# Kernel optimization log

Measured on AMD Instinct MI355X. Metric: run time of the kernel, lower is better.

The kernel has to match this reference:

```python
import jax, jax.numpy as jnp
import numpy as np
from jax import lax

B, C, H, W = 16, 128, 96, 96  # dim = C


def conv2d(x, w, b, pad, groups=1):
    y = lax.conv_general_dilated(
        x, w, window_strides=(1, 1), padding=[(pad, pad), (pad, pad)],
        dimension_numbers=("NCHW", "OIHW", "NCHW"), feature_group_count=groups)
    return y + b[None, :, None, None]


def setup_inputs() -> dict:
    key = jax.random.key(0)
    ks = jax.random.split(key, 16)
    std = 0.02
    inp = {
        "x": jax.random.normal(ks[0], (B, C, H, W), jnp.float32),
        "sin": jax.random.normal(ks[1], (H * W, C), jnp.float32),
        "cos": jax.random.normal(ks[2], (H * W, C), jnp.float32),
        # qkvo: 1x1 conv, dim -> 4*dim
        "w_qkvo": jax.random.normal(ks[3], (4 * C, C, 1, 1), jnp.float32) * std,
        "b_qkvo": jnp.zeros((4 * C,), jnp.float32),
        # lepe: 5x5 depthwise conv
        "w_lepe": jax.random.normal(ks[4], (C, 1, 5, 5), jnp.float32) * std,
        "b_lepe": jnp.zeros((C,), jnp.float32),
        # proj: 1x1 conv
        "w_proj": jax.random.normal(ks[5], (C, C, 1, 1), jnp.float32) * std,
        "b_proj": jnp.zeros((C,), jnp.float32),
        # 3x3 depthwise convs on q/k/v
        "w_q": jax.random.normal(ks[6], (C, 1, 3, 3), jnp.float32) * std,
        "b_q": jnp.zeros((C,), jnp.float32),
        "w_k": jax.random.normal(ks[7], (C, 1, 3, 3), jnp.float32) * std,
        "b_k": jnp.zeros((C,), jnp.float32),
        "w_v": jax.random.normal(ks[8], (C, 1, 3, 3), jnp.float32) * std,
        "b_v": jnp.zeros((C,), jnp.float32),
    }
    return inp


def reference(x, sin, cos, w_qkvo, b_qkvo, w_lepe, b_lepe, w_proj, b_proj,
              w_q, b_q, w_k, b_k, w_v, b_v):
    # sin/cos are accepted but unused, matching the original forward.
    b, c, h, w = x.shape
    hw = h * w
    scale = c ** (-0.5)

    qkvo = conv2d(x, w_qkvo, b_qkvo, 0)          # (B, 4C, H, W)
    qkv = qkvo[:, :3 * c]
    o = qkvo[:, 3 * c:]
    lepe = conv2d(qkv[:, 2 * c:], w_lepe, b_lepe, 2, groups=c)  # (B, C, H, W)

    q = qkv[:, :c]
    k = qkv[:, c:2 * c]
    v = qkv[:, 2 * c:]
    q = q + conv2d(q, w_q, b_q, 1, groups=c)
    k = k + conv2d(k, w_k, b_k, 1, groups=c)
    v = v + conv2d(v, w_v, b_v, 1, groups=c)

    # (B, C, H, W) -> (B, HW, C)
    to_tok = lambda t: t.reshape(b, c, hw).transpose(0, 2, 1)
    q = jax.nn.elu(to_tok(q)) + 1.0
    k = jax.nn.elu(to_tok(k)) + 1.0
    v = to_tok(v)

    k_mean = k.mean(axis=1, keepdims=True)                    # (B, 1, C)
    z = jnp.einsum("bnc,bmc->bnm", q, k_mean) * scale         # (B, HW, 1)

    s = (scale / hw) ** 0.5
    kv = jnp.einsum("bnc,bnd->bcd", k * s, v * s)             # (B, C, C)

    res = (jnp.einsum("bnc,bcd->bnd", q, kv) * (1.0 + 1.0 / (z + 1e-6))
           - z * v.mean(axis=2, keepdims=True))               # (B, HW, C)

    res = res.transpose(0, 2, 1).reshape(b, c, h, w)
    res = res + lepe
    return conv2d(res * o, w_proj, b_proj, 0)
```

## Files before the change

kernel.cpp:

```cpp
#include <hip/hip_runtime.h>
#include <math.h>

#define HW 9216
#define BSTRIDE_QKVO ((size_t)4718592)
#define BSTRIDE_C    ((size_t)1179648)
#define KVS 24

typedef __attribute__((ext_vector_type(4))) short short4v;
typedef __attribute__((ext_vector_type(8))) short short8v;
typedef __attribute__((ext_vector_type(4))) float f32x4;
typedef __attribute__((ext_vector_type(4))) unsigned short u16x4;

__device__ __forceinline__ unsigned short f2b(float f) {
  union { float f; unsigned u; } v; v.f = f;
  unsigned r = (v.u + 0x7fffu + ((v.u >> 16) & 1u)) >> 16;
  return (unsigned short)r;
}
__device__ __forceinline__ float b2f(unsigned short h) {
  union { unsigned u; float f; } v; v.u = ((unsigned)h) << 16;
  return v.f;
}

__global__ void cvt_kernel(const float* __restrict__ in, unsigned short* __restrict__ out, int n) {
  int i = blockIdx.x * 256 + threadIdx.x;
  if (i < n) out[i] = f2b(in[i]);
}

template<int BSRC_F32, int OUT_F32>
__global__ __launch_bounds__(256) void gemm_k128(
    const unsigned short* __restrict__ A, const void* __restrict__ Bv,
    const float* __restrict__ bias, void* __restrict__ Ov,
    size_t bstrB, size_t bstrO)
{
  __shared__ unsigned short Bt[128 * 132];
  const int t = threadIdx.x, lane = t & 63, wave = t >> 6;
  const int wr = wave >> 1, wc = wave & 1;
  const int l4 = lane & 15, lg = lane >> 4;
  const int pb = blockIdx.x << 7, ocb = blockIdx.y << 7, b = blockIdx.z;

  if (BSRC_F32) {
    const float* B = (const float*)Bv + (size_t)b * bstrB;
    #pragma unroll
    for (int i = 0; i < 8; ++i) {
      int id = t + (i << 8);
      int kp = id >> 5, pg = id & 31;
      const float* r0 = B + (size_t)(2 * kp) * HW + pb + (pg << 2);
      f32x4 a = *(const f32x4*)r0;
      f32x4 c = *(const f32x4*)(r0 + HW);
      #pragma unroll
      for (int j = 0; j < 4; ++j)
        *(unsigned*)&Bt[((pg << 2) + j) * 132 + 2 * kp] =
            (unsigned)f2b(a[j]) | ((unsigned)f2b(c[j]) << 16);
    }
  } else {
    const unsigned short* B = (const unsigned short*)Bv + (size_t)b * bstrB;
    #pragma unroll
    for (int i = 0; i < 8; ++i) {
      int id = t + (i << 8);
      int kp = id >> 5, pg = id & 31;
      const unsigned short* r0 = B + (size_t)(2 * kp) * HW + pb + (pg << 2);
      u16x4 a = *(const u16x4*)r0;
      u16x4 c = *(const u16x4*)(r0 + HW);
      #pragma unroll
      for (int j = 0; j < 4; ++j)
        *(unsigned*)&Bt[((pg << 2) + j) * 132 + 2 * kp] =
            (unsigned)a[j] | ((unsigned)c[j] << 16);
    }
  }

  short8v af[4][4];
  #pragma unroll
  for (int m = 0; m < 4; ++m)
    #pragma unroll
    for (int ks = 0; ks < 4; ++ks)
      af[m][ks] = *(const short8v*)(A + (size_t)(ocb + wr * 64 + m * 16 + l4) * 128 + ks * 32 + lg * 8);

  f32x4 acc[4][4];
  #pragma unroll
  for (int m = 0; m < 4; ++m)
    #pragma unroll
    for (int n = 0; n < 4; ++n) acc[m][n] = (f32x4){0.f, 0.f, 0.f, 0.f};

  __syncthreads();

  #pragma unroll
  for (int ks = 0; ks < 4; ++ks) {
    #pragma unroll
    for (int n = 0; n < 4; ++n) {
      int col = wc * 64 + n * 16 + l4;
      int base = col * 132 + ks * 32 + lg * 8;
      short4v lo = *(const short4v*)&Bt[base];
      short4v hi = *(const short4v*)&Bt[base + 4];
      short8v bfv;
      bfv[0] = lo[0]; bfv[1] = lo[1]; bfv[2] = lo[2]; bfv[3] = lo[3];
      bfv[4] = hi[0]; bfv[5] = hi[1]; bfv[6] = hi[2]; bfv[7] = hi[3];
      #pragma unroll
      for (int m = 0; m < 4; ++m)
        acc[m][n] = __builtin_amdgcn_mfma_f32_16x16x32_bf16(af[m][ks], bfv, acc[m][n], 0, 0, 0);
    }
  }

  float bs[4][4];
  #pragma unroll
  for (int m = 0; m < 4; ++m)
    #pragma unroll
    for (int i = 0; i < 4; ++i) bs[m][i] = bias[ocb + wr * 64 + m * 16 + lg * 4 + i];

  if (OUT_F32) {
    float* O = (float*)Ov + (size_t)b * bstrO;
    #pragma unroll
    for (int m = 0; m < 4; ++m)
      #pragma unroll
      for (int n = 0; n < 4; ++n) {
        int px = pb + wc * 64 + n * 16 + l4;
        #pragma unroll
        for (int i = 0; i < 4; ++i) {
          int oc = ocb + wr * 64 + m * 16 + lg * 4 + i;
          O[(size_t)oc * HW + px] = acc[m][n][i] + bs[m][i];
        }
      }
  } else {
    unsigned short* O = (unsigned short*)Ov + (size_t)b * bstrO;
    #pragma unroll
    for (int m = 0; m < 4; ++m)
      #pragma unroll
      for (int n = 0; n < 4; ++n) {
        int px = pb + wc * 64 + n * 16 + l4;
        #pragma unroll
        for (int i = 0; i < 4; ++i) {
          int oc = ocb + wr * 64 + m * 16 + lg * 4 + i;
          O[(size_t)oc * HW + px] = f2b(acc[m][n][i] + bs[m][i]);
        }
      }
  }
}

__device__ __forceinline__ void stage_plane(const unsigned short* __restrict__ g,
                                            float* __restrict__ sp, int t) {
  #pragma unroll
  for (int i = 0; i < 9; ++i) {
    int f = (t + (i << 8)) << 2;
    u16x4 u = *(const u16x4*)&g[f];
    f32x4 fv;
    fv[0] = b2f(u[0]); fv[1] = b2f(u[1]); fv[2] = b2f(u[2]); fv[3] = b2f(u[3]);
    *(f32x4*)&sp[f] = fv;
  }
}

__device__ __forceinline__ f32x4 conv3_strip(const float* __restrict__ sp, int base,
                                             const float* __restrict__ w9,
                                             bool j0, bool j23, f32x4* cen) {
  f32x4 acc = (f32x4){0.f, 0.f, 0.f, 0.f};
  #pragma unroll
  for (int ky = 0; ky < 3; ++ky) {
    const float* rowp = sp + base + (ky - 1) * 96;
    f32x4 w0 = *(const f32x4*)(rowp - 4);
    f32x4 w1 = *(const f32x4*)(rowp);
    f32x4 w2 = *(const f32x4*)(rowp + 4);
    float xm1 = j0 ? 0.f : w0[3];
    float xp4 = j23 ? 0.f : w2[0];
    float k0 = w9[ky * 3], k1 = w9[ky * 3 + 1], k2 = w9[ky * 3 + 2];
    acc[0] += k0 * xm1   + k1 * w1[0] + k2 * w1[1];
    acc[1] += k0 * w1[0] + k1 * w1[1] + k2 * w1[2];
    acc[2] += k0 * w1[1] + k1 * w1[2] + k2 * w1[3];
    acc[3] += k0 * w1[2] + k1 * w1[3] + k2 * xp4;
    if (ky == 1) *cen = w1;
  }
  return acc;
}

__global__ __launch_bounds__(256) void dwconv_kernel(
    unsigned short* __restrict__ qkvo,
    const float* __restrict__ w_q, const float* __restrict__ b_q,
    const float* __restrict__ w_k, const float* __restrict__ b_k,
    const float* __restrict__ w_v, const float* __restrict__ b_v,
    const float* __restrict__ w_lepe, const float* __restrict__ b_lepe,
    float* __restrict__ lp, float* __restrict__ ksum)
{
  __shared__ float sb[9612];
  __shared__ float red[256];
  const int c = blockIdx.x, b = blockIdx.y, t = threadIdx.x;
  unsigned short* qg = qkvo + ((size_t)b * 512 + c) * HW;
  unsigned short* kg = qg + (size_t)128 * HW;
  unsigned short* vg = qg + (size_t)256 * HW;
  float* lg = lp + ((size_t)b * 128 + c) * HW;
  float* sp = sb + 196;

  for (int i = t; i < 384; i += 256) {
    int idx = (i < 192) ? (i - 192) : (9024 + i);
    sp[idx] = 0.f;
  }

  {
    stage_plane(qg, sp, t);
    float w9[9];
    #pragma unroll
    for (int i = 0; i < 9; ++i) w9[i] = w_q[c * 9 + i];
    float bb = b_q[c];
    __syncthreads();
    for (int i = 0; i < 9; ++i) {
      int s = t + (i << 8);
      int r = s / 24, j = s - r * 24;
      int base = r * 96 + (j << 2);
      f32x4 cen;
      f32x4 a = conv3_strip(sp, base, w9, j == 0, j == 23, &cen);
      u16x4 o;
      #pragma unroll
      for (int k = 0; k < 4; ++k) {
        float v = cen[k] + bb + a[k];
        o[k] = f2b(v > 0.f ? v + 1.f : __expf(v));
      }
      *(u16x4*)&qg[base] = o;
    }
    __syncthreads();
  }
  float kacc = 0.f;
  {
    stage_plane(kg, sp, t);
    float w9[9];
    #pragma unroll
    for (int i = 0; i < 9; ++i) w9[i] = w_k[c * 9 + i];
    float bb = b_k[c];
    __syncthreads();
    for (int i = 0; i < 9; ++i) {
      int s = t + (i << 8);
      int r = s / 24, j = s - r * 24;
      int base = r * 96 + (j << 2);
      f32x4 cen;
      f32x4 a = conv3_strip(sp, base, w9, j == 0, j == 23, &cen);
      u16x4 o;
      #pragma unroll
      for (int k = 0; k < 4; ++k) {
        float v = cen[k] + bb + a[k];
        float e = v > 0.f ? v + 1.f : __expf(v);
        o[k] = f2b(e);
        kacc += e;
      }
      *(u16x4*)&kg[base] = o;
    }
    __syncthreads();
  }
  {
    stage_plane(vg, sp, t);
    float w9[9], w25[25];
    #pragma unroll
    for (int i = 0; i < 9; ++i) w9[i] = w_v[c * 9 + i];
    #pragma unroll
    for (int i = 0; i < 25; ++i) w25[i] = w_lepe[c * 25 + i];
    float bv = b_v[c], bl = b_lepe[c];
    __syncthreads();
    for (int i = 0; i < 9; ++i) {
      int s = t + (i << 8);
      int r = s / 24, j = s - r * 24;
      int base = r * 96 + (j << 2);
      bool j0 = (j == 0), j23 = (j == 23);
      f32x4 a3 = (f32x4){0.f, 0.f, 0.f, 0.f};
      f32x4 a5 = (f32x4){0.f, 0.f, 0.f, 0.f};
      f32x4 cen = (f32x4){0.f, 0.f, 0.f, 0.f};
      #pragma unroll
      for (int ky = 0; ky < 5; ++ky) {
        const float* rowp = sp + base + (ky - 2) * 96;
        f32x4 w0 = *(const f32x4*)(rowp - 4);
        f32x4 w1 = *(const f32x4*)(rowp);
        f32x4 w2 = *(const f32x4*)(rowp + 4);
        float xm2 = j0 ? 0.f : w0[2];
        float xm1 = j0 ? 0.f : w0[3];
        float xp4 = j23 ? 0.f : w2[0];
        float xp5 = j23 ? 0.f : w2[1];
        const float* wr5 = w25 + ky * 5;
        a5[0] += wr5[0]*xm2   + wr5[1]*xm1   + wr5[2]*w1[0] + wr5[3]*w1[1] + wr5[4]*w1[2];
        a5[1] += wr5[0]*xm1   + wr5[1]*w1[0] + wr5[2]*w1[1] + wr5[3]*w1[2] + wr5[4]*w1[3];
        a5[2] += wr5[0]*w1[0] + wr5[1]*w1[1] + wr5[2]*w1[2] + wr5[3]*w1[3] + wr5[4]*xp4;
        a5[3] += wr5[0]*w1[1] + wr5[1]*w1[2] + wr5[2]*w1[3] + wr5[3]*xp4   + wr5[4]*xp5;
        if (ky >= 1 && ky <= 3) {
          float k0 = w9[(ky-1)*3], k1 = w9[(ky-1)*3+1], k2 = w9[(ky-1)*3+2];
          a3[0] += k0 * xm1   + k1 * w1[0] + k2 * w1[1];
          a3[1] += k0 * w1[0] + k1 * w1[1] + k2 * w1[2];
          a3[2] += k0 * w1[1] + k1 * w1[2] + k2 * w1[3];
          a3[3] += k0 * w1[2] + k1 * w1[3] + k2 * xp4;
          if (ky == 2) cen = w1;
        }
      }
      u16x4 o;
      f32x4 lout;
      #pragma unroll
      for (int k = 0; k < 4; ++k) {
        o[k] = f2b(cen[k] + bv + a3[k]);
        lout[k] = bl + a5[k];
      }
      *(u16x4*)&vg[base] = o;
      *(f32x4*)&lg[base] = lout;
    }
  }
  red[t] = kacc; __syncthreads();
  for (int s2 = 128; s2 > 0; s2 >>= 1) { if (t < s2) red[t] += red[t + s2]; __syncthreads(); }
  if (t == 0) ksum[b * 128 + c] = red[0];
}

__global__ __launch_bounds__(256) void kv_mfma(
    const unsigned short* __restrict__ qkvo, float* __restrict__ part)
{
  const int t = threadIdx.x, lane = t & 63, wave = t >> 6;
  const int wr = wave >> 1, wc = wave & 1;
  const int l4 = lane & 15, lg = lane >> 4;
  const int s = blockIdx.x, b = blockIdx.y;
  const unsigned short* kbase = qkvo + (size_t)b * BSTRIDE_QKVO + (size_t)128 * HW;
  const unsigned short* vbase = kbase + (size_t)128 * HW;
  const int p0 = s * 384;

  f32x4 acc[4][4];
  #pragma unroll
  for (int m = 0; m < 4; ++m)
    #pragma unroll
    for (int n = 0; n < 4; ++n) acc[m][n] = (f32x4){0.f, 0.f, 0.f, 0.f};

  for (int kk = 0; kk < 12; ++kk) {
    int p = p0 + kk * 32 + lg * 8;
    short8v ka[4], va[4];
    #pragma unroll
    for (int m = 0; m < 4; ++m) ka[m] = *(const short8v*)(kbase + (size_t)(wr * 64 + m * 16 + l4) * HW + p);
    #pragma unroll
    for (int n = 0; n < 4; ++n) va[n] = *(const short8v*)(vbase + (size_t)(wc * 64 + n * 16 + l4) * HW + p);
    #pragma unroll
    for (int n = 0; n < 4; ++n)
      #pragma unroll
      for (int m = 0; m < 4; ++m)
        acc[m][n] = __builtin_amdgcn_mfma_f32_16x16x32_bf16(ka[m], va[n], acc[m][n], 0, 0, 0);
  }

  float* pp = part + ((size_t)b * KVS + s) * 16384;
  #pragma unroll
  for (int m = 0; m < 4; ++m)
    #pragma unroll
    for (int n = 0; n < 4; ++n) {
      int d = wc * 64 + n * 16 + l4;
      #pragma unroll
      for (int i = 0; i < 4; ++i) {
        int cch = wr * 64 + m * 16 + lg * 4 + i;
        pp[(cch << 7) + d] = acc[m][n][i];
      }
    }
}

__global__ void kvreduce(const float* __restrict__ part, unsigned short* __restrict__ kvT) {
  const int b = blockIdx.y;
  const int e0 = blockIdx.x * 2048 + threadIdx.x;
  const float* pb_ = part + (size_t)b * KVS * 16384;
  for (int i = 0; i < 8; ++i) {
    int e = e0 + i * 256;
    int cch = e >> 7, d = e & 127;
    float sum = 0.f;
    #pragma unroll 8
    for (int s = 0; s < KVS; ++s) sum += pb_[(size_t)s * 16384 + e];
    kvT[(size_t)b * 16384 + d * 128 + cch] = f2b(sum);
  }
}

__global__ void vmean_k(const unsigned short* __restrict__ qkvo, float* __restrict__ vmean) {
  const int b = blockIdx.y;
  const int px = blockIdx.x * 256 + threadIdx.x;
  const unsigned short* vb = qkvo + (size_t)b * BSTRIDE_QKVO + (size_t)256 * HW + px;
  float s = 0.f;
  #pragma unroll 8
  for (int d = 0; d < 128; ++d) s += b2f(vb[(size_t)d * HW]);
  vmean[(size_t)b * HW + px] = s * (1.f / 128.f);
}

__global__ __launch_bounds__(256) void attn_mfma(
    unsigned short* __restrict__ qkvo, const unsigned short* __restrict__ kvT,
    const float* __restrict__ ksum, const float* __restrict__ vmean,
    const float* __restrict__ lp)
{
  __shared__ unsigned short Bt[128 * 132];
  __shared__ float zb[128];
  __shared__ float km[128];
  const int t = threadIdx.x, lane = t & 63, wave = t >> 6;
  const int wr = wave >> 1, wc = wave & 1;
  const int l4 = lane & 15, lg = lane >> 4;
  const int pb = blockIdx.x << 7, b = blockIdx.y;
  const float kSCf = (float)(0.08838834764831843 / 9216.0);

  unsigned short* qs = qkvo + (size_t)b * BSTRIDE_QKVO;
  const unsigned short* os = qs + (size_t)384 * HW;
  const float* lpb = lp + (size_t)b * BSTRIDE_C;

  if (t < 128) km[t] = ksum[(b << 7) + t];

  #pragma unroll
  for (int i = 0; i < 8; ++i) {
    int id = t + (i << 8);
    int kp = id >> 5, pg = id & 31;
    const unsigned short* r0 = qs + (size_t)(2 * kp) * HW + pb + (pg << 2);
    u16x4 a = *(const u16x4*)r0;
    u16x4 c = *(const u16x4*)(r0 + HW);
    #pragma unroll
    for (int j = 0; j < 4; ++j)
      *(unsigned*)&Bt[((pg << 2) + j) * 132 + 2 * kp] =
          (unsigned)a[j] | ((unsigned)c[j] << 16);
  }

  const unsigned short* Ab = kvT + (size_t)b * 16384;
  short8v af[4][4];
  #pragma unroll
  for (int m = 0; m < 4; ++m)
    #pragma unroll
    for (int ks = 0; ks < 4; ++ks)
      af[m][ks] = *(const short8v*)(Ab + (size_t)(wr * 64 + m * 16 + l4) * 128 + ks * 32 + lg * 8);

  f32x4 acc[4][4];
  #pragma unroll
  for (int m = 0; m < 4; ++m)
    #pragma unroll
    for (int n = 0; n < 4; ++n) acc[m][n] = (f32x4){0.f, 0.f, 0.f, 0.f};

  __syncthreads();

  if (t < 128) {
    float za = 0.f;
    #pragma unroll 8
    for (int cch = 0; cch < 128; ++cch) za += b2f(Bt[t * 132 + cch]) * km[cch];
    zb[t] = za;
  }

  #pragma unroll
  for (int ks = 0; ks < 4; ++ks) {
    #pragma unroll
    for (int n = 0; n < 4; ++n) {
      int col = wc * 64 + n * 16 + l4;
      int base = col * 132 + ks * 32 + lg * 8;
      short4v lo = *(const short4v*)&Bt[base];
      short4v hi = *(const short4v*)&Bt[base + 4];
      short8v bfv;
      bfv[0] = lo[0]; bfv[1] = lo[1]; bfv[2] = lo[2]; bfv[3] = lo[3];
      bfv[4] = hi[0]; bfv[5] = hi[1]; bfv[6] = hi[2]; bfv[7] = hi[3];
      #pragma unroll
      for (int m = 0; m < 4; ++m)
        acc[m][n] = __builtin_amdgcn_mfma_f32_16x16x32_bf16(af[m][ks], bfv, acc[m][n], 0, 0, 0);
    }
  }

  __syncthreads();

  #pragma unroll
  for (int n = 0; n < 4; ++n) {
    int pxl = wc * 64 + n * 16 + l4;
    int px = pb + pxl;
    float z  = zb[pxl] * kSCf;
    float zf = kSCf * (1.f + 1.f / (z + 1e-6f));
    float zvm = z * vmean[(size_t)b * HW + px];
    #pragma unroll
    for (int m = 0; m < 4; ++m)
      #pragma unroll
      for (int i = 0; i < 4; ++i) {
        int d = wr * 64 + m * 16 + lg * 4 + i;
        float le = lpb[(size_t)d * HW + px];
        float ov = b2f(os[(size_t)d * HW + px]);
        float r = (acc[m][n][i] * zf - zvm + le) * ov;
        qs[(size_t)d * HW + px] = f2b(r);
      }
  }
}

extern "C" void kernel_launch(void* const* d_in, const int* in_sizes, int n_in,
                              void* d_out, int out_size, void* d_ws, size_t ws_size,
                              hipStream_t stream) {
  const float* x      = (const float*)d_in[0];
  const float* w_qkvo = (const float*)d_in[3];
  const float* b_qkvo = (const float*)d_in[4];
  const float* w_lepe = (const float*)d_in[5];
  const float* b_lepe = (const float*)d_in[6];
  const float* w_proj = (const float*)d_in[7];
  const float* b_proj = (const float*)d_in[8];
  const float* w_q = (const float*)d_in[9];
  const float* b_q = (const float*)d_in[10];
  const float* w_k = (const float*)d_in[11];
  const float* b_k = (const float*)d_in[12];
  const float* w_v = (const float*)d_in[13];
  const float* b_v = (const float*)d_in[14];
  float* out = (float*)d_out;

  unsigned short* wqh = (unsigned short*)d_ws;
  unsigned short* wph = wqh + 65536;
  const size_t perb_bytes = 9437184 + 1572864 + 32768 + 512 + 36864;
  int G = 0;
  for (int g = 16; g >= 1; g >>= 1)
    if ((size_t)163840 + (size_t)g * perb_bytes <= ws_size) { G = g; break; }
  if (G == 0) return;

  size_t off = 163840;
  unsigned short* qkvo_h = (unsigned short*)((char*)d_ws + off); off += (size_t)G * 9437184;
  float* kvpart = (float*)((char*)d_ws + off);                   off += (size_t)G * 1572864;
  unsigned short* kvT = (unsigned short*)((char*)d_ws + off);    off += (size_t)G * 32768;
  float* ksum = (float*)((char*)d_ws + off);                     off += (size_t)G * 512;
  float* vmeanp = (float*)((char*)d_ws + off);

  cvt_kernel<<<dim3(256), 256, 0, stream>>>(w_qkvo, wqh, 65536);
  cvt_kernel<<<dim3(64),  256, 0, stream>>>(w_proj, wph, 16384);

  for (int b0 = 0; b0 < 16; b0 += G) {
    const float* xc  = x   + (size_t)b0 * BSTRIDE_C;
    float*       oc_ = out + (size_t)b0 * BSTRIDE_C;

    gemm_k128<1, 0><<<dim3(72, 4, G), 256, 0, stream>>>(
        wqh, xc, b_qkvo, qkvo_h, BSTRIDE_C, BSTRIDE_QKVO);
    dwconv_kernel<<<dim3(128, G), 256, 0, stream>>>(qkvo_h, w_q, b_q, w_k, b_k, w_v, b_v,
                                                    w_lepe, b_lepe, oc_, ksum);
    kv_mfma<<<dim3(KVS, G), 256, 0, stream>>>(qkvo_h, kvpart);
    kvreduce<<<dim3(8, G), 256, 0, stream>>>(kvpart, kvT);
    vmean_k<<<dim3(36, G), 256, 0, stream>>>(qkvo_h, vmeanp);
    attn_mfma<<<dim3(72, G), 256, 0, stream>>>(qkvo_h, kvT, ksum, vmeanp, oc_);
    gemm_k128<0, 1><<<dim3(72, 1, G), 256, 0, stream>>>(
        wph, qkvo_h, b_proj, oc_, BSTRIDE_QKVO, BSTRIDE_C);
  }
}
```

Before: 324.3 us.

## Swap MFMA operand roles so pixels are rows and stores vectorize; reuse staged tile across output blocks

The GEMM kernel now puts the staged input tile (pixels) in the A operand and the weights in the B operand. Each lane then holds 4 consecutive pixels, so outputs are written as f32x4/u16x4 vector stores instead of scalar strided ones. The qkvo GEMM loops over all 4 output-channel blocks inside one workgroup, so the converted x tile is staged once rather than four times, at the cost of a quarter as many blocks. The attention epilogue gets the same transpose, which vectorizes its lepe, o, vmean and z loads and its stores.

Result: faster. 299.4 us (-7.7%).

```diff
diff --git a/kernel.cpp b/kernel.cpp
--- a/kernel.cpp
+++ b/kernel.cpp
@@ -26,8 +26,8 @@
   if (i < n) out[i] = f2b(in[i]);
 }
 
-template<int BSRC_F32, int OUT_F32>
-__global__ __launch_bounds__(256) void gemm_k128(
+template<int BSRC_F32, int OUT_F32, int NOCB>
+__global__ __launch_bounds__(256) void gemm_k128s(
     const unsigned short* __restrict__ A, const void* __restrict__ Bv,
     const float* __restrict__ bias, void* __restrict__ Ov,
     size_t bstrB, size_t bstrO)
@@ -36,7 +36,7 @@
   const int t = threadIdx.x, lane = t & 63, wave = t >> 6;
   const int wr = wave >> 1, wc = wave & 1;
   const int l4 = lane & 15, lg = lane >> 4;
-  const int pb = blockIdx.x << 7, ocb = blockIdx.y << 7, b = blockIdx.z;
+  const int pb = blockIdx.x << 7, b = blockIdx.y;
 
   if (BSRC_F32) {
     const float* B = (const float*)Bv + (size_t)b * bstrB;
@@ -68,70 +68,75 @@
     }
   }
 
+  __syncthreads();
+
   short8v af[4][4];
   #pragma unroll
-  for (int m = 0; m < 4; ++m)
-    #pragma unroll
-    for (int ks = 0; ks < 4; ++ks)
-      af[m][ks] = *(const short8v*)(A + (size_t)(ocb + wr * 64 + m * 16 + l4) * 128 + ks * 32 + lg * 8);
-
-  f32x4 acc[4][4];
-  #pragma unroll
-  for (int m = 0; m < 4; ++m)
-    #pragma unroll
-    for (int n = 0; n < 4; ++n) acc[m][n] = (f32x4){0.f, 0.f, 0.f, 0.f};
-
-  __syncthreads();
-
-  #pragma unroll
-  for (int ks = 0; ks < 4; ++ks) {
-    #pragma unroll
-    for (int n = 0; n < 4; ++n) {
-      int col = wc * 64 + n * 16 + l4;
-      int base = col * 132 + ks * 32 + lg * 8;
+  for (int mp = 0; mp < 4; ++mp)
+    #pragma unroll
+    for (int ks = 0; ks < 4; ++ks) {
+      int base = (wr * 64 + mp * 16 + l4) * 132 + ks * 32 + lg * 8;
       short4v lo = *(const short4v*)&Bt[base];
       short4v hi = *(const short4v*)&Bt[base + 4];
-      short8v bfv;
-      bfv[0] = lo[0]; bfv[1] = lo[1]; bfv[2] = lo[2]; bfv[3] = lo[3];
-      bfv[4] = hi[0]; bfv[5] = hi[1]; bfv[6] = hi[2]; bfv[7] = hi[3];
-      #pragma unroll
-      for (int m = 0; m < 4; ++m)
-        acc[m][n] = __builtin_amdgcn_mfma_f32_16x16x32_bf16(af[m][ks], bfv, acc[m][n], 0, 0, 0);
-    }
-  }
-
-  float bs[4][4];
-  #pragma unroll
-  for (int m = 0; m < 4; ++m)
-    #pragma unroll
-    for (int i = 0; i < 4; ++i) bs[m][i] = bias[ocb + wr * 64 + m * 16 + lg * 4 + i];
-
-  if (OUT_F32) {
-    float* O = (float*)Ov + (size_t)b * bstrO;
-    #pragma unroll
-    for (int m = 0; m < 4; ++m)
-      #pragma unroll
-      for (int n = 0; n < 4; ++n) {
-        int px = pb + wc * 64 + n * 16 + l4;
+      short8v v;
+      v[0] = lo[0]; v[1] = lo[1]; v[2] = lo[2]; v[3] = lo[3];
+      v[4] = hi[0]; v[5] = hi[1]; v[6] = hi[2]; v[7] = hi[3];
+      af[mp][ks] = v;
+    }
+
+  for (int co = 0; co < NOCB; ++co) {
+    f32x4 acc[4][4];
+    #pragma unroll
+    for (int mp = 0; mp < 4; ++mp)
+      #pragma unroll
+      for (int nd = 0; nd < 4; ++nd) acc[mp][nd] = (f32x4){0.f, 0.f, 0.f, 0.f};
+
+    #pragma unroll
+    for (int ks = 0; ks < 4; ++ks) {
+      short8v bfk[4];
+      #pragma unroll
+      for (int nd = 0; nd < 4; ++nd)
+        bfk[nd] = *(const short8v*)(A + (size_t)(co * 128 + wc * 64 + nd * 16 + l4) * 128 + ks * 32 + lg * 8);
+      #pragma unroll
+      for (int nd = 0; nd < 4; ++nd)
         #pragma unroll
-        for (int i = 0; i < 4; ++i) {
-          int oc = ocb + wr * 64 + m * 16 + lg * 4 + i;
-          O[(size_t)oc * HW + px] = acc[m][n][i] + bs[m][i];
+        for (int mp = 0; mp < 4; ++mp)
+          acc[mp][nd] = __builtin_amdgcn_mfma_f32_16x16x32_bf16(af[mp][ks], bfk[nd], acc[mp][nd], 0, 0, 0);
+    }
+
+    float bb[4];
+    #pragma unroll
+    for (int nd = 0; nd < 4; ++nd) bb[nd] = bias[co * 128 + wc * 64 + nd * 16 + l4];
+
+    if (OUT_F32) {
+      float* O = (float*)Ov + (size_t)b * bstrO;
+      #pragma unroll
+      for (int mp = 0; mp < 4; ++mp) {
+        int px = pb + wr * 64 + mp * 16 + lg * 4;
+        #pragma unroll
+        for (int nd = 0; nd < 4; ++nd) {
+          int oc = co * 128 + wc * 64 + nd * 16 + l4;
+          f32x4 v;
+          #pragma unroll
+          for (int i = 0; i < 4; ++i) v[i] = acc[mp][nd][i] + bb[nd];
+          *(f32x4*)&O[(size_t)oc * HW + px] = v;
         }
       }
-  } else {
-    unsigned short* O = (unsigned short*)Ov + (size_t)b * bstrO;
-    #pragma unroll
-    for (int m = 0; m < 4; ++m)
-      #pragma unroll
-      for (int n = 0; n < 4; ++n) {
-        int px = pb + wc * 64 + n * 16 + l4;
+    } else {
+      unsigned short* O = (unsigned short*)Ov + (size_t)b * bstrO;
+      #pragma unroll
+      for (int mp = 0; mp < 4; ++mp) {
+        int px = pb + wr * 64 + mp * 16 + lg * 4;
         #pragma unroll
-        for (int i = 0; i < 4; ++i) {
-          int oc = ocb + wr * 64 + m * 16 + lg * 4 + i;
-          O[(size_t)oc * HW + px] = f2b(acc[m][n][i] + bs[m][i]);
+        for (int nd = 0; nd < 4; ++nd) {
+          int oc = co * 128 + wc * 64 + nd * 16 + l4;
+          u16x4 v;
+          #pragma unroll
+          for (int i = 0; i < 4; ++i) v[i] = f2b(acc[mp][nd][i] + bb[nd]);
+          *(u16x4*)&O[(size_t)oc * HW + px] = v;
         }
       }
+    }
   }
 }
 
@@ -400,18 +405,18 @@
   }
 
   const unsigned short* Ab = kvT + (size_t)b * 16384;
-  short8v af[4][4];
-  #pragma unroll
-  for (int m = 0; m < 4; ++m)
+  short8v bkv[4][4];
+  #pragma unroll
+  for (int nd = 0; nd < 4; ++nd)
     #pragma unroll
     for (int ks = 0; ks < 4; ++ks)
-      af[m][ks] = *(const short8v*)(Ab + (size_t)(wr * 64 + m * 16 + l4) * 128 + ks * 32 + lg * 8);
+      bkv[nd][ks] = *(const short8v*)(Ab + (size_t)(wc * 64 + nd * 16 + l4) * 128 + ks * 32 + lg * 8);
 
   f32x4 acc[4][4];
   #pragma unroll
-  for (int m = 0; m < 4; ++m)
-    #pragma unroll
-    for (int n = 0; n < 4; ++n) acc[m][n] = (f32x4){0.f, 0.f, 0.f, 0.f};
+  for (int mp = 0; mp < 4; ++mp)
+    #pragma unroll
+    for (int nd = 0; nd < 4; ++nd) acc[mp][nd] = (f32x4){0.f, 0.f, 0.f, 0.f};
 
   __syncthreads();
 
@@ -424,40 +429,52 @@
 
   #pragma unroll
   for (int ks = 0; ks < 4; ++ks) {
-    #pragma unroll
-    for (int n = 0; n < 4; ++n) {
-      int col = wc * 64 + n * 16 + l4;
-      int base = col * 132 + ks * 32 + lg * 8;
+    short8v aq[4];
+    #pragma unroll
+    for (int mp = 0; mp < 4; ++mp) {
+      int base = (wr * 64 + mp * 16 + l4) * 132 + ks * 32 + lg * 8;
       short4v lo = *(const short4v*)&Bt[base];
       short4v hi = *(const short4v*)&Bt[base + 4];
-      short8v bfv;
-      bfv[0] = lo[0]; bfv[1] = lo[1]; bfv[2] = lo[2]; bfv[3] = lo[3];
-      bfv[4] = hi[0]; bfv[5] = hi[1]; bfv[6] = hi[2]; bfv[7] = hi[3];
-      #pragma unroll
-      for (int m = 0; m < 4; ++m)
-        acc[m][n] = __builtin_amdgcn_mfma_f32_16x16x32_bf16(af[m][ks], bfv, acc[m][n], 0, 0, 0);
-    }
+      short8v v;
+      v[0] = lo[0]; v[1] = lo[1]; v[2] = lo[2]; v[3] = lo[3];
+      v[4] = hi[0]; v[5] = hi[1]; v[6] = hi[2]; v[7] = hi[3];
+      aq[mp] = v;
+    }
+    #pragma unroll
+    for (int nd = 0; nd < 4; ++nd)
+      #pragma unroll
+      for (int mp = 0; mp < 4; ++mp)
+        acc[mp][nd] = __builtin_amdgcn_mfma_f32_16x16x32_bf16(aq[mp], bkv[nd][ks], acc[mp][nd], 0, 0, 0);
   }
 
   __syncthreads();
 
   #pragma unroll
-  for (int n = 0; n < 4; ++n) {
-    int pxl = wc * 64 + n * 16 + l4;
+  for (int mp = 0; mp < 4; ++mp) {
+    int pxl = wr * 64 + mp * 16 + lg * 4;
     int px = pb + pxl;
-    float z  = zb[pxl] * kSCf;
-    float zf = kSCf * (1.f + 1.f / (z + 1e-6f));
-    float zvm = z * vmean[(size_t)b * HW + px];
-    #pragma unroll
-    for (int m = 0; m < 4; ++m)
+    f32x4 zv = *(const f32x4*)&zb[pxl];
+    f32x4 vm = *(const f32x4*)&vmean[(size_t)b * HW + px];
+    f32x4 zfv, zvmv;
+    #pragma unroll
+    for (int i = 0; i < 4; ++i) {
+      float z = zv[i] * kSCf;
+      zfv[i]  = kSCf * (1.f + 1.f / (z + 1e-6f));
+      zvmv[i] = z * vm[i];
+    }
+    #pragma unroll
+    for (int nd = 0; nd < 4; ++nd) {
+      int d = wc * 64 + nd * 16 + l4;
+      f32x4 le = *(const f32x4*)&lpb[(size_t)d * HW + px];
+      u16x4 ovv = *(const u16x4*)&os[(size_t)d * HW + px];
+      u16x4 o;
       #pragma unroll
       for (int i = 0; i < 4; ++i) {
-        int d = wr * 64 + m * 16 + lg * 4 + i;
-        float le = lpb[(size_t)d * HW + px];
-        float ov = b2f(os[(size_t)d * HW + px]);
-        float r = (acc[m][n][i] * zf - zvm + le) * ov;
-        qs[(size_t)d * HW + px] = f2b(r);
-      }
+        float r = (acc[mp][nd][i] * zfv[i] - zvmv[i] + le[i]) * b2f(ovv[i]);
+        o[i] = f2b(r);
+      }
+      *(u16x4*)&qs[(size_t)d * HW + px] = o;
+    }
   }
 }
 
@@ -501,7 +518,7 @@
     const float* xc  = x   + (size_t)b0 * BSTRIDE_C;
     float*       oc_ = out + (size_t)b0 * BSTRIDE_C;
 
-    gemm_k128<1, 0><<<dim3(72, 4, G), 256, 0, stream>>>(
+    gemm_k128s<1, 0, 4><<<dim3(72, G), 256, 0, stream>>>(
         wqh, xc, b_qkvo, qkvo_h, BSTRIDE_C, BSTRIDE_QKVO);
     dwconv_kernel<<<dim3(128, G), 256, 0, stream>>>(qkvo_h, w_q, b_q, w_k, b_k, w_v, b_v,
                                                     w_lepe, b_lepe, oc_, ksum);
@@ -509,7 +526,7 @@
     kvreduce<<<dim3(8, G), 256, 0, stream>>>(kvpart, kvT);
     vmean_k<<<dim3(36, G), 256, 0, stream>>>(qkvo_h, vmeanp);
     attn_mfma<<<dim3(72, G), 256, 0, stream>>>(qkvo_h, kvT, ksum, vmeanp, oc_);
-    gemm_k128<0, 1><<<dim3(72, 1, G), 256, 0, stream>>>(
+    gemm_k128s<0, 1, 1><<<dim3(72, G), 256, 0, stream>>>(
         wph, qkvo_h, b_proj, oc_, BSTRIDE_QKVO, BSTRIDE_C);
   }
 }
```
